# Performance work log

Measured on AMD Instinct MI355X. Metric: run time of the kernel, lower is better.

## Reference

```python
import jax, jax.numpy as jnp
import numpy as np

NUM_EVAL_NEGATIVES = 999  # rconst.NUM_EVAL_NEGATIVES
ROW = NUM_EVAL_NEGATIVES + 1  # 1000 candidates per user (1 positive + 999 negatives)
TOP_K = 10                # rconst.TOP_K
NUM_USERS = 8192


def setup_inputs() -> dict:
    key = jax.random.key(0)
    k1, k2 = jax.random.split(key)
    logits = jax.random.normal(k1, (NUM_USERS * ROW, 1, 2), dtype=jnp.float32)
    dup_mask = jax.random.randint(k2, (NUM_USERS * ROW, 1, 1), 0, 2, dtype=jnp.int32)
    return {"logits": logits, "dup_mask": dup_mask}


def reference(logits, dup_mask):
    # metric_fn: cast mask to float, slice off channel 0 of the softmax pair
    dup = dup_mask.astype(jnp.float32)
    l = logits[:, :, 1:]

    # compute_top_k_and_ndcg (match_mlperf=True)
    logits_by_user = l.reshape(-1, ROW)            # [U, 1000]
    dup_by_user = dup.reshape(-1, ROW)             # [U, 1000]

    # mask duplicate candidates to dtype min
    big_neg = jnp.finfo(logits_by_user.dtype).min
    logits_by_user = logits_by_user * (1.0 - dup_by_user) + dup_by_user * big_neg

    # descending argsort; position of the true item (index 0) in the ranking
    sort_indices = jnp.argsort(-logits_by_user, axis=1)  # [U, 1000]
    ranks = jnp.arange(ROW, dtype=logits_by_user.dtype)  # [1000]
    position_vector = jnp.sum(
        (sort_indices == 0).astype(logits_by_user.dtype) * ranks, axis=1)  # [U]

    in_top_k = (position_vector < TOP_K).astype(jnp.float32)
    ndcg = jnp.log(2.0) / jnp.log(position_vector + 2.0) * in_top_k

    # padded rows: all negatives are duplicates
    metric_weights = (jnp.sum(dup_by_user, axis=1) != NUM_EVAL_NEGATIVES).astype(jnp.float32)

    return in_top_k, ndcg, metric_weights
```

## Files before the change

kernel.cpp:

```cpp
#include <hip/hip_runtime.h>
#include <hip/hip_bf16.h>
#include <float.h>

#define ROW 1000
#define SLOTS (ROW / 4)
#define TOP_K 10
#define NUM_EVAL_NEG 999
#define USERS_PER_BLOCK 4

typedef float vfloat4 __attribute__((ext_vector_type(4)));
typedef int   vint4   __attribute__((ext_vector_type(4)));

__global__ __launch_bounds__(256) void metric_kernel(
    const float* __restrict__ logits,
    const int*   __restrict__ dup,
    float* __restrict__ out,
    int num_users)
{
    const int tid  = threadIdx.x;
    const int lane = tid & 63;
    const int user = blockIdx.x * USERS_PER_BLOCK + (tid >> 6);
    if (user >= num_users) return;

    const float BIG_NEG = -FLT_MAX;
    const long long base = (long long)user * ROW;

    const int   d0 = dup[base];
    const float l0 = logits[2 * base + 1];
    const float x0 = d0 ? BIG_NEG : l0;

    const vfloat4* lg4 = reinterpret_cast<const vfloat4*>(logits + 2 * base);
    const vint4*   dp4 = reinterpret_cast<const vint4*>(dup + base);

    int cnt = 0;
    int dsum = 0;

    #pragma unroll 2
    for (int s = lane; s < SLOTS; s += 64) {
        vfloat4 a = lg4[2 * s];
        vfloat4 b = lg4[2 * s + 1];
        vint4   d = dp4[s];
        cnt += (d.x == 0 && a.y > x0) ? 1 : 0;
        cnt += (d.y == 0 && a.w > x0) ? 1 : 0;
        cnt += (d.z == 0 && b.y > x0) ? 1 : 0;
        cnt += (d.w == 0 && b.w > x0) ? 1 : 0;
        dsum += d.x + d.y + d.z + d.w;
    }

    #pragma unroll
    for (int off = 32; off > 0; off >>= 1) {
        cnt  += __shfl_down(cnt, off, 64);
        dsum += __shfl_down(dsum, off, 64);
    }

    if (lane == 0) {
        float pos  = (float)cnt;
        float itk  = (pos < (float)TOP_K) ? 1.0f : 0.0f;
        float ndcg = (itk != 0.0f) ? (0.69314718055994530942f / logf(pos + 2.0f)) : 0.0f;
        float w    = (dsum != NUM_EVAL_NEG) ? 1.0f : 0.0f;
        out[user]                 = itk;
        out[num_users + user]     = ndcg;
        out[2 * num_users + user] = w;
    }
}

extern "C" void kernel_launch(void* const* d_in, const int* in_sizes, int n_in,
                              void* d_out, int out_size, void* d_ws, size_t ws_size,
                              hipStream_t stream) {
    const float* logits = (const float*)d_in[0];
    const int*   dup    = (const int*)d_in[1];
    float* out = (float*)d_out;

    const int num_users = in_sizes[0] / (2 * ROW);
    const int grid = (num_users + USERS_PER_BLOCK - 1) / USERS_PER_BLOCK;

    metric_kernel<<<grid, 256, 0, stream>>>(logits, dup, out, num_users);
}
```

Measured before the change: 110.4 us.

## Use contiguous per-lane logit loads with wave ballots and bitmask dup matching

Each lane now reads consecutive 16-byte logit chunks, so a wave's loads are fully contiguous instead of strided pairs. The per-element comparisons are packed into 64-bit ballot masks. A second pass loads the dup words and uses shifted mask bits to subtract the comparisons that hit duplicates. This aims for better coalescing and fully unrolled loads, at the cost of extra ballots, bit work and clamped redundant loads for the tail lanes.

```diff
diff --git a/kernel.cpp b/kernel.cpp
--- a/kernel.cpp
+++ b/kernel.cpp
@@ -1,9 +1,9 @@
 #include <hip/hip_runtime.h>
-#include <hip/hip_bf16.h>
 #include <float.h>
 
 #define ROW 1000
-#define SLOTS (ROW / 4)
+#define CHUNKS_L 500
+#define CHUNKS_D 250
 #define TOP_K 10
 #define NUM_EVAL_NEG 999
 #define USERS_PER_BLOCK 4
@@ -32,32 +32,51 @@
     const vfloat4* lg4 = reinterpret_cast<const vfloat4*>(logits + 2 * base);
     const vint4*   dp4 = reinterpret_cast<const vint4*>(dup + base);
 
-    int cnt = 0;
-    int dsum = 0;
+    unsigned long long be[8], bo[8];
+    #pragma unroll
+    for (int k = 0; k < 8; ++k) {
+        const int c  = 64 * k + lane;
+        const int cc = (c < CHUNKS_L) ? c : (CHUNKS_L - 1);
+        const vfloat4 a = lg4[cc];
+        const bool valid = (c < CHUNKS_L);
+        be[k] = __ballot(valid && (a.y > x0));
+        bo[k] = __ballot(valid && (a.w > x0));
+    }
 
-    #pragma unroll 2
-    for (int s = lane; s < SLOTS; s += 64) {
-        vfloat4 a = lg4[2 * s];
-        vfloat4 b = lg4[2 * s + 1];
-        vint4   d = dp4[s];
-        cnt += (d.x == 0 && a.y > x0) ? 1 : 0;
-        cnt += (d.y == 0 && a.w > x0) ? 1 : 0;
-        cnt += (d.z == 0 && b.y > x0) ? 1 : 0;
-        cnt += (d.w == 0 && b.w > x0) ? 1 : 0;
-        dsum += d.x + d.y + d.z + d.w;
+    int cnt1 = 0;
+    #pragma unroll
+    for (int k = 0; k < 8; ++k)
+        cnt1 += __popcll(be[k]) + __popcll(bo[k]);
+
+    int cross = 0, dsum = 0;
+    const int  i  = (2 * lane) & 63;
+    const bool hi = (lane & 32) != 0;
+    #pragma unroll
+    for (int m = 0; m < 4; ++m) {
+        const int g  = 64 * m + lane;
+        const int gc = (g < CHUNKS_D) ? g : (CHUNKS_D - 1);
+        const vint4 d = dp4[gc];
+        const int v = (g < CHUNKS_D) ? 1 : 0;
+        const unsigned long long we = hi ? be[2*m + 1] : be[2*m];
+        const unsigned long long wo = hi ? bo[2*m + 1] : bo[2*m];
+        const unsigned re = (unsigned)(we >> i);
+        const unsigned ro = (unsigned)(wo >> i);
+        cross += v * ((d.x & re & 1) + (d.y & ro & 1)
+                    + ((d.z & (re >> 1)) & 1) + ((d.w & (ro >> 1)) & 1));
+        dsum  += v * (d.x + d.y + d.z + d.w);
     }
 
     #pragma unroll
     for (int off = 32; off > 0; off >>= 1) {
-        cnt  += __shfl_down(cnt, off, 64);
-        dsum += __shfl_down(dsum, off, 64);
+        cross += __shfl_down(cross, off, 64);
+        dsum  += __shfl_down(dsum, off, 64);
     }
 
     if (lane == 0) {
-        float pos  = (float)cnt;
-        float itk  = (pos < (float)TOP_K) ? 1.0f : 0.0f;
-        float ndcg = (itk != 0.0f) ? (0.69314718055994530942f / logf(pos + 2.0f)) : 0.0f;
-        float w    = (dsum != NUM_EVAL_NEG) ? 1.0f : 0.0f;
+        const float pos  = (float)(cnt1 - cross);
+        const float itk  = (pos < (float)TOP_K) ? 1.0f : 0.0f;
+        const float ndcg = (itk != 0.0f) ? (0.69314718055994530942f / logf(pos + 2.0f)) : 0.0f;
+        const float w    = (dsum != NUM_EVAL_NEG) ? 1.0f : 0.0f;
         out[user]                 = itk;
         out[num_users + user]     = ndcg;
         out[2 * num_users + user] = w;
```

Measured after the change: 137.6 us. 24.6% more time.
